# Kernel optimization log

Hardware: AMD Instinct MI355X
Metric: run time of the kernel (lower is better)

The kernel has to match this reference:

```python
import jax, jax.numpy as jnp
import numpy as np

N = 50000  # total nodes


def sage_conv(x, src, dst, Wl, Wr, b):
    # PyG SAGEConv with mean aggregation: out = mean_{j in N(i)} x_j @ Wl + x_i @ Wr + b
    agg = jax.ops.segment_sum(x[src], dst, num_segments=N)
    deg = jax.ops.segment_sum(jnp.ones((src.shape[0],), x.dtype), dst, num_segments=N)
    mean = agg / jnp.maximum(deg, 1.0)[:, None]
    return mean @ Wl + x @ Wr + b


def setup_inputs() -> dict:
    key = jax.random.key(0)
    ks = jax.random.split(key, 16)
    F_in, D, H, B, E1, E2, A = 128, 64, 128, 16, 800000, 200000, 2000
    s = lambda fan: 1.0 / np.sqrt(fan)
    return {
        "x": jax.random.normal(ks[0], (N, F_in), jnp.float32),
        "edge_index": jax.random.randint(ks[1], (2, E1), 0, N),
        "new_edges": jax.random.randint(ks[2], (B, 2, E2), 0, N),
        "target_nodes": jax.random.randint(ks[3], (B,), 0, N),
        "regions": jax.random.randint(ks[4], (B, A), 0, N),
        "W1l": jax.random.normal(ks[5], (F_in, D), jnp.float32) * s(F_in),
        "W1r": jax.random.normal(ks[6], (F_in, D), jnp.float32) * s(F_in),
        "b1": jnp.zeros((D,), jnp.float32),
        "W2l": jax.random.normal(ks[7], (D, D), jnp.float32) * s(D),
        "W2r": jax.random.normal(ks[8], (D, D), jnp.float32) * s(D),
        "b2": jnp.zeros((D,), jnp.float32),
        "Wm": jax.random.normal(ks[9], (D, H), jnp.float32) * s(D),
        "bm": jnp.zeros((H,), jnp.float32),
        "Wo": jax.random.normal(ks[10], (H, D), jnp.float32) * s(H),
        "bo": jnp.zeros((D,), jnp.float32),
    }


def reference(x, edge_index, new_edges, target_nodes, regions,
              W1l, W1r, b1, W2l, W2r, b2, Wm, bm, Wo, bo):
    # shared conv1 over base graph
    h1 = jax.nn.relu(sage_conv(x, edge_index[0], edge_index[1], W1l, W1r, b1))  # [N,D]

    def per_graph(edges, t, region):
        h2 = jax.nn.relu(sage_conv(h1, edges[0], edges[1], W2l, W2r, b2))  # [N,D]
        target_embed = h2[t]          # [D]
        region_embed = h2[region]     # [A,D]
        e = jax.nn.relu(region_embed @ Wm + bm)  # [A,H]
        r = e @ Wo + bo                           # [A,D]
        return r @ target_embed                   # [A]  (bilin_q)

    q = jax.vmap(per_graph)(new_edges, target_nodes, regions)  # [B,A]
    return q
```

## Files before the change

### kernel.cpp

```cpp
#include <hip/hip_runtime.h>
#include <hip/hip_bf16.h>

#define NN 50000
#define E1C 800000
#define E2C 200000
#define BC 16
#define AC 2000
#define FIN 128
#define DD 64
#define HH 128
#define SLOTS (AC + 1)
#define SCAP 64
#define SCAP2 32
#define NPART 8
#define PSZ (NN / NPART)

__global__ __launch_bounds__(256, 2) void k_lin1(const float* __restrict__ x,
    const float* __restrict__ W1l, const float* __restrict__ W1r,
    const float* __restrict__ b1,
    float* __restrict__ y, float* __restrict__ z) {
  __shared__ __align__(16) float Wsh[FIN][FIN];
  __shared__ __align__(16) float xr2[32][FIN];
  for (int i = threadIdx.x; i < FIN * FIN; i += 256) {
    int k = i >> 7, c = i & 127;
    Wsh[k][c] = (c < DD) ? W1l[k * DD + c] : W1r[k * DD + (c - DD)];
  }
  const int cg = threadIdx.x & 31, c0 = cg * 4;
  const int rg = threadIdx.x >> 5, r0 = rg * 4;
  float4 bias = make_float4(0.f, 0.f, 0.f, 0.f);
  if (cg >= 16) bias = *(const float4*)(b1 + c0 - DD);
  const int ntiles = (NN + 31) / 32;
  for (int t = blockIdx.x; t < ntiles; t += gridDim.x) {
    int base = t * 32;
    __syncthreads();
#pragma unroll
    for (int p = 0; p < 4; ++p) {
      int row = p * 8 + (threadIdx.x >> 5);
      int k0 = (threadIdx.x & 31) * 4;
      int gr = base + row;
      float4 v = (gr < NN) ? *(const float4*)(x + (size_t)gr * FIN + k0)
                           : make_float4(0.f, 0.f, 0.f, 0.f);
      *(float4*)&xr2[row][k0] = v;
    }
    __syncthreads();
    float acc[4][4] = {};
#pragma unroll 4
    for (int kk = 0; kk < FIN; kk += 4) {
      float4 xq0 = *(const float4*)&xr2[r0 + 0][kk];
      float4 xq1 = *(const float4*)&xr2[r0 + 1][kk];
      float4 xq2 = *(const float4*)&xr2[r0 + 2][kk];
      float4 xq3 = *(const float4*)&xr2[r0 + 3][kk];
#pragma unroll
      for (int j = 0; j < 4; ++j) {
        float4 wv = *(const float4*)&Wsh[kk + j][c0];
        float x0 = (j == 0) ? xq0.x : (j == 1) ? xq0.y : (j == 2) ? xq0.z : xq0.w;
        float x1 = (j == 0) ? xq1.x : (j == 1) ? xq1.y : (j == 2) ? xq1.z : xq1.w;
        float x2 = (j == 0) ? xq2.x : (j == 1) ? xq2.y : (j == 2) ? xq2.z : xq2.w;
        float x3 = (j == 0) ? xq3.x : (j == 1) ? xq3.y : (j == 2) ? xq3.z : xq3.w;
        acc[0][0] = fmaf(x0, wv.x, acc[0][0]); acc[0][1] = fmaf(x0, wv.y, acc[0][1]);
        acc[0][2] = fmaf(x0, wv.z, acc[0][2]); acc[0][3] = fmaf(x0, wv.w, acc[0][3]);
        acc[1][0] = fmaf(x1, wv.x, acc[1][0]); acc[1][1] = fmaf(x1, wv.y, acc[1][1]);
        acc[1][2] = fmaf(x1, wv.z, acc[1][2]); acc[1][3] = fmaf(x1, wv.w, acc[1][3]);
        acc[2][0] = fmaf(x2, wv.x, acc[2][0]); acc[2][1] = fmaf(x2, wv.y, acc[2][1]);
        acc[2][2] = fmaf(x2, wv.z, acc[2][2]); acc[2][3] = fmaf(x2, wv.w, acc[2][3]);
        acc[3][0] = fmaf(x3, wv.x, acc[3][0]); acc[3][1] = fmaf(x3, wv.y, acc[3][1]);
        acc[3][2] = fmaf(x3, wv.z, acc[3][2]); acc[3][3] = fmaf(x3, wv.w, acc[3][3]);
      }
    }
#pragma unroll
    for (int i = 0; i < 4; ++i) {
      int gr = base + r0 + i;
      if (gr < NN) {
        float4 o = make_float4(acc[i][0] + bias.x, acc[i][1] + bias.y,
                               acc[i][2] + bias.z, acc[i][3] + bias.w);
        if (cg < 16) *(float4*)(y + (size_t)gr * DD + c0) = o;
        else         *(float4*)(z + (size_t)gr * DD + (c0 - DD)) = o;
      }
    }
  }
}

__global__ __launch_bounds__(256) void k_degslot(const int* __restrict__ src,
    const int* __restrict__ dst, int* __restrict__ degi, int* __restrict__ slots) {
  int part = blockIdx.x & (NPART - 1);
  int lb   = blockIdx.x >> 3;
  int nlb  = gridDim.x >> 3;
  int lo = part * PSZ, hi = lo + PSZ;
  for (int e = lb * 256 + threadIdx.x; e < E1C; e += nlb * 256) {
    int d = dst[e];
    if (d >= lo && d < hi) {
      int p = atomicAdd(&degi[d], 1);
      if (p < SCAP) slots[(size_t)d * SCAP + p] = src[e];
    }
  }
}

__global__ __launch_bounds__(256) void k_gather_h1(const int* __restrict__ degi,
    const int* __restrict__ slots, const float* __restrict__ y,
    const float* __restrict__ z, float* __restrict__ h1) {
  int w = blockIdx.x * 4 + (threadIdx.x >> 6);
  int lane = threadIdx.x & 63;
  if (w >= NN) return;
  int deg = degi[w];
  int n = min(deg, SCAP);
  const int* sp = slots + (size_t)w * SCAP;
  float acc = 0.f;
  int j = 0;
  for (; j + 4 <= n; j += 4) {
    int s0 = sp[j], s1 = sp[j + 1], s2 = sp[j + 2], s3 = sp[j + 3];
    float a0 = y[(size_t)s0 * DD + lane];
    float a1 = y[(size_t)s1 * DD + lane];
    float a2 = y[(size_t)s2 * DD + lane];
    float a3 = y[(size_t)s3 * DD + lane];
    acc += (a0 + a1) + (a2 + a3);
  }
  for (; j < n; ++j) acc += y[(size_t)sp[j] * DD + lane];
  float m = acc / fmaxf((float)deg, 1.f);
  h1[(size_t)w * DD + lane] = fmaxf(m + z[(size_t)w * DD + lane], 0.f);
}

__global__ __launch_bounds__(256, 2) void k_lin2(const float* __restrict__ h1,
    const float* __restrict__ W2l, const float* __restrict__ W2r,
    const float* __restrict__ b2,
    float* __restrict__ u, float* __restrict__ v) {
  __shared__ __align__(16) float Wsh[DD][128];
  __shared__ __align__(16) float xr2[32][DD];
  for (int i = threadIdx.x; i < DD * 128; i += 256) {
    int k = i >> 7, c = i & 127;
    Wsh[k][c] = (c < DD) ? W2l[k * DD + c] : W2r[k * DD + (c - DD)];
  }
  const int cg = threadIdx.x & 31, c0 = cg * 4;
  const int rg = threadIdx.x >> 5, r0 = rg * 4;
  float4 bias = make_float4(0.f, 0.f, 0.f, 0.f);
  if (cg >= 16) bias = *(const float4*)(b2 + c0 - DD);
  const int ntiles = (NN + 31) / 32;
  for (int t = blockIdx.x; t < ntiles; t += gridDim.x) {
    int base = t * 32;
    __syncthreads();
#pragma unroll
    for (int p = 0; p < 2; ++p) {
      int row = p * 16 + (threadIdx.x >> 4);
      int k0 = (threadIdx.x & 15) * 4;
      int gr = base + row;
      float4 vv = (gr < NN) ? *(const float4*)(h1 + (size_t)gr * DD + k0)
                            : make_float4(0.f, 0.f, 0.f, 0.f);
      *(float4*)&xr2[row][k0] = vv;
    }
    __syncthreads();
    float acc[4][4] = {};
#pragma unroll 4
    for (int kk = 0; kk < DD; kk += 4) {
      float4 xq0 = *(const float4*)&xr2[r0 + 0][kk];
      float4 xq1 = *(const float4*)&xr2[r0 + 1][kk];
      float4 xq2 = *(const float4*)&xr2[r0 + 2][kk];
      float4 xq3 = *(const float4*)&xr2[r0 + 3][kk];
#pragma unroll
      for (int j = 0; j < 4; ++j) {
        float4 wv = *(const float4*)&Wsh[kk + j][c0];
        float x0 = (j == 0) ? xq0.x : (j == 1) ? xq0.y : (j == 2) ? xq0.z : xq0.w;
        float x1 = (j == 0) ? xq1.x : (j == 1) ? xq1.y : (j == 2) ? xq1.z : xq1.w;
        float x2 = (j == 0) ? xq2.x : (j == 1) ? xq2.y : (j == 2) ? xq2.z : xq2.w;
        float x3 = (j == 0) ? xq3.x : (j == 1) ? xq3.y : (j == 2) ? xq3.z : xq3.w;
        acc[0][0] = fmaf(x0, wv.x, acc[0][0]); acc[0][1] = fmaf(x0, wv.y, acc[0][1]);
        acc[0][2] = fmaf(x0, wv.z, acc[0][2]); acc[0][3] = fmaf(x0, wv.w, acc[0][3]);
        acc[1][0] = fmaf(x1, wv.x, acc[1][0]); acc[1][1] = fmaf(x1, wv.y, acc[1][1]);
        acc[1][2] = fmaf(x1, wv.z, acc[1][2]); acc[1][3] = fmaf(x1, wv.w, acc[1][3]);
        acc[2][0] = fmaf(x2, wv.x, acc[2][0]); acc[2][1] = fmaf(x2, wv.y, acc[2][1]);
        acc[2][2] = fmaf(x2, wv.z, acc[2][2]); acc[2][3] = fmaf(x2, wv.w, acc[2][3]);
        acc[3][0] = fmaf(x3, wv.x, acc[3][0]); acc[3][1] = fmaf(x3, wv.y, acc[3][1]);
        acc[3][2] = fmaf(x3, wv.z, acc[3][2]); acc[3][3] = fmaf(x3, wv.w, acc[3][3]);
      }
    }
#pragma unroll
    for (int i = 0; i < 4; ++i) {
      int gr = base + r0 + i;
      if (gr < NN) {
        float4 o = make_float4(acc[i][0] + bias.x, acc[i][1] + bias.y,
                               acc[i][2] + bias.z, acc[i][3] + bias.w);
        if (cg < 16) *(float4*)(u + (size_t)gr * DD + c0) = o;
        else         *(float4*)(v + (size_t)gr * DD + (c0 - DD)) = o;
      }
    }
  }
}

__global__ void k_mark(const int* __restrict__ regions, const int* __restrict__ targets,
                       int* __restrict__ mark, int* __restrict__ rep) {
  int i = blockIdx.x * blockDim.x + threadIdx.x;
  if (i >= BC * SLOTS) return;
  int b = i / SLOTS, k = i % SLOTS;
  int node = (k < AC) ? regions[b * AC + k] : targets[b];
  int old = atomicCAS(&mark[b * NN + node], -1, k);
  rep[i] = (old < 0) ? k : old;
}

__global__ void k_filter(const int* __restrict__ ne, const int* __restrict__ mark,
                         int* __restrict__ deg2i, int* __restrict__ slots2) {
  int e = blockIdx.x * blockDim.x + threadIdx.x;
  int b = blockIdx.y;
  if (e >= E2C) return;
  int d = ne[b * 2 * E2C + E2C + e];
  int k = mark[b * NN + d];
  if (k >= 0) {
    int s = ne[b * 2 * E2C + e];
    int p = atomicAdd(&deg2i[b * SLOTS + k], 1);
    if (p < SCAP2) slots2[((size_t)b * SLOTS + k) * SCAP2 + p] = s;
  }
}

__global__ __launch_bounds__(256) void k_gather_h2(const int* __restrict__ deg2i,
    const int* __restrict__ slots2, const int* __restrict__ rep,
    const int* __restrict__ regions, const int* __restrict__ targets,
    const float* __restrict__ u, const float* __restrict__ v,
    float* __restrict__ h2c) {
  int w = blockIdx.x * 4 + (threadIdx.x >> 6);
  int lane = threadIdx.x & 63;
  if (w >= BC * SLOTS) return;
  int b = w / SLOTS, k = w - b * SLOTS;
  int r = rep[w];
  int deg = deg2i[b * SLOTS + r];
  int n = min(deg, SCAP2);
  const int* sp = slots2 + ((size_t)b * SLOTS + r) * SCAP2;
  float acc = 0.f;
  int j = 0;
  for (; j + 4 <= n; j += 4) {
    int s0 = sp[j], s1 = sp[j + 1], s2 = sp[j + 2], s3 = sp[j + 3];
    float a0 = u[(size_t)s0 * DD + lane];
    float a1 = u[(size_t)s1 * DD + lane];
    float a2 = u[(size_t)s2 * DD + lane];
    float a3 = u[(size_t)s3 * DD + lane];
    acc += (a0 + a1) + (a2 + a3);
  }
  for (; j < n; ++j) acc += u[(size_t)sp[j] * DD + lane];
  int node = (k < AC) ? regions[b * AC + k] : targets[b];
  float m = acc / fmaxf((float)deg, 1.f);
  h2c[(size_t)w * DD + lane] = fmaxf(m + v[(size_t)node * DD + lane], 0.f);
}

__global__ void k_wt(const float* __restrict__ h2c, const float* __restrict__ Wo,
                     const float* __restrict__ bo, float* __restrict__ wt,
                     float* __restrict__ c0) {
  int b = blockIdx.x;
  int t = threadIdx.x;
  __shared__ float te[DD];
  if (t < DD) te[t] = h2c[((size_t)b * SLOTS + AC) * DD + t];
  __syncthreads();
  float acc = 0.f;
#pragma unroll
  for (int d = 0; d < DD; ++d) acc = fmaf(Wo[t * DD + d], te[d], acc);
  wt[b * HH + t] = acc;
  if (t == 0) {
    float s = 0.f;
    for (int d = 0; d < DD; ++d) s += bo[d] * te[d];
    c0[b] = s;
  }
}

__global__ __launch_bounds__(256) void k_q(const float* __restrict__ h2c,
    const float* __restrict__ Wm, const float* __restrict__ bm,
    const float* __restrict__ wt, const float* __restrict__ c0,
    float* __restrict__ q) {
  __shared__ float W[DD][HH];
  __shared__ float bmL[HH], wtL[HH];
  int b = blockIdx.y;
  for (int i = threadIdx.x; i < DD * HH; i += 256) W[i >> 7][i & 127] = Wm[i];
  if (threadIdx.x < HH) {
    bmL[threadIdx.x] = bm[threadIdx.x];
    wtL[threadIdx.x] = wt[b * HH + threadIdx.x];
  }
  __syncthreads();
  float cc = c0[b];
  int lane = threadIdx.x & 63;
  int wv = threadIdx.x >> 6;
  int nwv = (blockDim.x >> 6) * gridDim.x;
  for (int a = blockIdx.x * 4 + wv; a < AC; a += nwv) {
    float hv = h2c[((size_t)b * SLOTS + a) * DD + lane];
    float a0 = 0.f, a1 = 0.f;
#pragma unroll
    for (int d = 0; d < DD; ++d) {
      float xd = __shfl(hv, d);
      a0 = fmaf(xd, W[d][lane], a0);
      a1 = fmaf(xd, W[d][lane + 64], a1);
    }
    float e0 = fmaxf(a0 + bmL[lane], 0.f);
    float e1 = fmaxf(a1 + bmL[lane + 64], 0.f);
    float p = fmaf(e0, wtL[lane], e1 * wtL[lane + 64]);
#pragma unroll
    for (int m = 32; m; m >>= 1) p += __shfl_xor(p, m);
    if (lane == 0) q[b * AC + a] = p + cc;
  }
}

extern "C" void kernel_launch(void* const* d_in, const int* in_sizes, int n_in,
                              void* d_out, int out_size, void* d_ws, size_t ws_size,
                              hipStream_t stream) {
  const float* x    = (const float*)d_in[0];
  const int*   ei   = (const int*)d_in[1];
  const int*   ne   = (const int*)d_in[2];
  const int*   tgt  = (const int*)d_in[3];
  const int*   reg  = (const int*)d_in[4];
  const float* W1l  = (const float*)d_in[5];
  const float* W1r  = (const float*)d_in[6];
  const float* b1   = (const float*)d_in[7];
  const float* W2l  = (const float*)d_in[8];
  const float* W2r  = (const float*)d_in[9];
  const float* b2   = (const float*)d_in[10];
  const float* Wm   = (const float*)d_in[11];
  const float* bm   = (const float*)d_in[12];
  const float* Wo   = (const float*)d_in[13];
  const float* bo   = (const float*)d_in[14];
  float* q = (float*)d_out;

  char* w = (char*)d_ws;
  size_t off = 0;
  auto alloc = [&](size_t bytes) { void* p = w + off; off = (off + bytes + 255) & ~(size_t)255; return p; };
  float* y_u   = (float*)alloc((size_t)NN * DD * 4);
  float* z_v   = (float*)alloc((size_t)NN * DD * 4);
  float* h1b   = (float*)alloc((size_t)NN * DD * 4);
  int*   degi  = (int*)alloc((size_t)NN * 4);
  int*   slots = (int*)alloc((size_t)NN * SCAP * 4);
  int*   mark  = (int*)alloc((size_t)BC * NN * 4);
  int*   rep   = (int*)alloc((size_t)BC * SLOTS * 4);
  int*   deg2i = (int*)alloc((size_t)BC * SLOTS * 4);
  int*   slots2= (int*)alloc((size_t)BC * SLOTS * SCAP2 * 4);
  float* h2c   = (float*)alloc((size_t)BC * SLOTS * DD * 4);
  float* wt    = (float*)alloc((size_t)BC * HH * 4);
  float* c0    = (float*)alloc(64);
  (void)ws_size; (void)n_in; (void)in_sizes; (void)out_size;

  hipMemsetAsync(degi,  0,    (size_t)NN * 4, stream);
  hipMemsetAsync(mark,  0xFF, (size_t)BC * NN * 4, stream);
  hipMemsetAsync(deg2i, 0,    (size_t)BC * SLOTS * 4, stream);

  const int* e_src = ei;
  const int* e_dst = ei + E1C;

  k_lin1<<<512, 256, 0, stream>>>(x, W1l, W1r, b1, y_u, z_v);
  k_degslot<<<2048, 256, 0, stream>>>(e_src, e_dst, degi, slots);
  k_gather_h1<<<(NN + 3) / 4, 256, 0, stream>>>(degi, slots, y_u, z_v, h1b);
  k_lin2<<<512, 256, 0, stream>>>(h1b, W2l, W2r, b2, y_u, z_v);
  k_mark<<<(BC * SLOTS + 255) / 256, 256, 0, stream>>>(reg, tgt, mark, rep);
  k_filter<<<dim3((E2C + 255) / 256, BC), 256, 0, stream>>>(ne, mark, deg2i, slots2);
  k_gather_h2<<<(BC * SLOTS + 3) / 4, 256, 0, stream>>>(deg2i, slots2, rep, reg, tgt,
                                                        y_u, z_v, h2c);
  k_wt<<<BC, 128, 0, stream>>>(h2c, Wo, bo, wt, c0);
  k_q<<<dim3(32, BC), 256, 0, stream>>>(h2c, Wm, bm, wt, c0, q);
}
```

Baseline: 320.7 us.

## Merge independent kernels into combined launches and drop LDS staging in linears

Result: no change. 317.9 us (-0.9%).

```diff
diff --git a/kernel.cpp b/kernel.cpp
--- a/kernel.cpp
+++ b/kernel.cpp
@@ -14,13 +14,17 @@
 #define SCAP2 32
 #define NPART 8
 #define PSZ (NN / NPART)
+#define DEGB 2048
+#define MARKB ((BC * SLOTS + 255) / 256)
+#define GH1B ((NN + 3) / 4)
+#define FILTB 196
+#define Q_NBLK 32
 
 __global__ __launch_bounds__(256, 2) void k_lin1(const float* __restrict__ x,
     const float* __restrict__ W1l, const float* __restrict__ W1r,
     const float* __restrict__ b1,
     float* __restrict__ y, float* __restrict__ z) {
   __shared__ __align__(16) float Wsh[FIN][FIN];
-  __shared__ __align__(16) float xr2[32][FIN];
   for (int i = threadIdx.x; i < FIN * FIN; i += 256) {
     int k = i >> 7, c = i & 127;
     Wsh[k][c] = (c < DD) ? W1l[k * DD + c] : W1r[k * DD + (c - DD)];
@@ -29,27 +33,22 @@
   const int rg = threadIdx.x >> 5, r0 = rg * 4;
   float4 bias = make_float4(0.f, 0.f, 0.f, 0.f);
   if (cg >= 16) bias = *(const float4*)(b1 + c0 - DD);
+  __syncthreads();
   const int ntiles = (NN + 31) / 32;
   for (int t = blockIdx.x; t < ntiles; t += gridDim.x) {
     int base = t * 32;
-    __syncthreads();
-#pragma unroll
-    for (int p = 0; p < 4; ++p) {
-      int row = p * 8 + (threadIdx.x >> 5);
-      int k0 = (threadIdx.x & 31) * 4;
-      int gr = base + row;
-      float4 v = (gr < NN) ? *(const float4*)(x + (size_t)gr * FIN + k0)
-                           : make_float4(0.f, 0.f, 0.f, 0.f);
-      *(float4*)&xr2[row][k0] = v;
-    }
-    __syncthreads();
+    int gr0 = base + r0;
+    const float* xp0 = x + (size_t)min(gr0 + 0, NN - 1) * FIN;
+    const float* xp1 = x + (size_t)min(gr0 + 1, NN - 1) * FIN;
+    const float* xp2 = x + (size_t)min(gr0 + 2, NN - 1) * FIN;
+    const float* xp3 = x + (size_t)min(gr0 + 3, NN - 1) * FIN;
     float acc[4][4] = {};
 #pragma unroll 4
     for (int kk = 0; kk < FIN; kk += 4) {
-      float4 xq0 = *(const float4*)&xr2[r0 + 0][kk];
-      float4 xq1 = *(const float4*)&xr2[r0 + 1][kk];
-      float4 xq2 = *(const float4*)&xr2[r0 + 2][kk];
-      float4 xq3 = *(const float4*)&xr2[r0 + 3][kk];
+      float4 xq0 = *(const float4*)(xp0 + kk);
+      float4 xq1 = *(const float4*)(xp1 + kk);
+      float4 xq2 = *(const float4*)(xp2 + kk);
+      float4 xq3 = *(const float4*)(xp3 + kk);
 #pragma unroll
       for (int j = 0; j < 4; ++j) {
         float4 wv = *(const float4*)&Wsh[kk + j][c0];
@@ -80,51 +79,83 @@
   }
 }
 
-__global__ __launch_bounds__(256) void k_degslot(const int* __restrict__ src,
-    const int* __restrict__ dst, int* __restrict__ degi, int* __restrict__ slots) {
-  int part = blockIdx.x & (NPART - 1);
-  int lb   = blockIdx.x >> 3;
-  int nlb  = gridDim.x >> 3;
-  int lo = part * PSZ, hi = lo + PSZ;
-  for (int e = lb * 256 + threadIdx.x; e < E1C; e += nlb * 256) {
-    int d = dst[e];
-    if (d >= lo && d < hi) {
-      int p = atomicAdd(&degi[d], 1);
-      if (p < SCAP) slots[(size_t)d * SCAP + p] = src[e];
-    }
-  }
-}
-
-__global__ __launch_bounds__(256) void k_gather_h1(const int* __restrict__ degi,
+__global__ __launch_bounds__(256) void k_prep(const int* __restrict__ src,
+    const int* __restrict__ dst, int* __restrict__ degi, int* __restrict__ slots,
+    const int* __restrict__ regions, const int* __restrict__ targets,
+    int* __restrict__ mark, int* __restrict__ rep) {
+  if (blockIdx.x < DEGB) {
+    int part = blockIdx.x & (NPART - 1);
+    int lb   = blockIdx.x >> 3;
+    int nlb  = DEGB >> 3;
+    int lo = part * PSZ, hi = lo + PSZ;
+    for (int e = lb * 256 + threadIdx.x; e < E1C; e += nlb * 256) {
+      int d = dst[e];
+      if (d >= lo && d < hi) {
+        int p = atomicAdd(&degi[d], 1);
+        if (p < SCAP) slots[(size_t)d * SCAP + p] = src[e];
+      }
+    }
+  } else {
+    int i = (blockIdx.x - DEGB) * 256 + threadIdx.x;
+    if (i >= BC * SLOTS) return;
+    int b = i / SLOTS, k = i % SLOTS;
+    int node = (k < AC) ? regions[b * AC + k] : targets[b];
+    int old = atomicCAS(&mark[b * NN + node], -1, k);
+    rep[i] = (old < 0) ? k : old;
+  }
+}
+
+__global__ __launch_bounds__(256) void k_sparse2(const int* __restrict__ degi,
     const int* __restrict__ slots, const float* __restrict__ y,
-    const float* __restrict__ z, float* __restrict__ h1) {
-  int w = blockIdx.x * 4 + (threadIdx.x >> 6);
-  int lane = threadIdx.x & 63;
-  if (w >= NN) return;
-  int deg = degi[w];
-  int n = min(deg, SCAP);
-  const int* sp = slots + (size_t)w * SCAP;
-  float acc = 0.f;
-  int j = 0;
-  for (; j + 4 <= n; j += 4) {
-    int s0 = sp[j], s1 = sp[j + 1], s2 = sp[j + 2], s3 = sp[j + 3];
-    float a0 = y[(size_t)s0 * DD + lane];
-    float a1 = y[(size_t)s1 * DD + lane];
-    float a2 = y[(size_t)s2 * DD + lane];
-    float a3 = y[(size_t)s3 * DD + lane];
-    acc += (a0 + a1) + (a2 + a3);
-  }
-  for (; j < n; ++j) acc += y[(size_t)sp[j] * DD + lane];
-  float m = acc / fmaxf((float)deg, 1.f);
-  h1[(size_t)w * DD + lane] = fmaxf(m + z[(size_t)w * DD + lane], 0.f);
-}
-
-__global__ __launch_bounds__(256, 2) void k_lin2(const float* __restrict__ h1,
+    const float* __restrict__ z, float* __restrict__ h1,
+    const int* __restrict__ ne, const int* __restrict__ mark,
+    int* __restrict__ deg2i, int* __restrict__ slots2) {
+  if (blockIdx.x < GH1B) {
+    int w = blockIdx.x * 4 + (threadIdx.x >> 6);
+    int lane = threadIdx.x & 63;
+    if (w >= NN) return;
+    int deg = degi[w];
+    int n = min(deg, SCAP);
+    const int* sp = slots + (size_t)w * SCAP;
+    float acc = 0.f;
+    int j = 0;
+    for (; j + 4 <= n; j += 4) {
+      int s0 = sp[j], s1 = sp[j + 1], s2 = sp[j + 2], s3 = sp[j + 3];
+      float a0 = y[(size_t)s0 * DD + lane];
+      float a1 = y[(size_t)s1 * DD + lane];
+      float a2 = y[(size_t)s2 * DD + lane];
+      float a3 = y[(size_t)s3 * DD + lane];
+      acc += (a0 + a1) + (a2 + a3);
+    }
+    for (; j < n; ++j) acc += y[(size_t)sp[j] * DD + lane];
+    float m = acc / fmaxf((float)deg, 1.f);
+    h1[(size_t)w * DD + lane] = fmaxf(m + z[(size_t)w * DD + lane], 0.f);
+  } else {
+    int fid = blockIdx.x - GH1B;
+    int b = fid / FILTB, eb = fid % FILTB;
+    int e = eb * 1024 + threadIdx.x * 4;
+    if (e >= E2C) return;
+    const int* srcp = ne + (size_t)b * 2 * E2C;
+    const int* dstp = srcp + E2C;
+    int4 d4 = *(const int4*)(dstp + e);
+    const int* mb = mark + (size_t)b * NN;
+    int k0 = mb[d4.x], k1 = mb[d4.y], k2 = mb[d4.z], k3 = mb[d4.w];
+    if (k0 >= 0) { int p = atomicAdd(&deg2i[b * SLOTS + k0], 1);
+      if (p < SCAP2) slots2[((size_t)b * SLOTS + k0) * SCAP2 + p] = srcp[e]; }
+    if (k1 >= 0) { int p = atomicAdd(&deg2i[b * SLOTS + k1], 1);
+      if (p < SCAP2) slots2[((size_t)b * SLOTS + k1) * SCAP2 + p] = srcp[e + 1]; }
+    if (k2 >= 0) { int p = atomicAdd(&deg2i[b * SLOTS + k2], 1);
+      if (p < SCAP2) slots2[((size_t)b * SLOTS + k2) * SCAP2 + p] = srcp[e + 2]; }
+    if (k3 >= 0) { int p = atomicAdd(&deg2i[b * SLOTS + k3], 1);
+      if (p < SCAP2) slots2[((size_t)b * SLOTS + k3) * SCAP2 + p] = srcp[e + 3]; }
+  }
+}
+
+__global__ __launch_bounds__(256, 4) void k_lin2(const float* __restrict__ h1,
     const float* __restrict__ W2l, const float* __restrict__ W2r,
     const float* __restrict__ b2,
     float* __restrict__ u, float* __restrict__ v) {
   __shared__ __align__(16) float Wsh[DD][128];
-  __shared__ __align__(16) float xr2[32][DD];
   for (int i = threadIdx.x; i < DD * 128; i += 256) {
     int k = i >> 7, c = i & 127;
     Wsh[k][c] = (c < DD) ? W2l[k * DD + c] : W2r[k * DD + (c - DD)];
@@ -133,27 +164,22 @@
   const int rg = threadIdx.x >> 5, r0 = rg * 4;
   float4 bias = make_float4(0.f, 0.f, 0.f, 0.f);
   if (cg >= 16) bias = *(const float4*)(b2 + c0 - DD);
+  __syncthreads();
   const int ntiles = (NN + 31) / 32;
   for (int t = blockIdx.x; t < ntiles; t += gridDim.x) {
     int base = t * 32;
-    __syncthreads();
-#pragma unroll
-    for (int p = 0; p < 2; ++p) {
-      int row = p * 16 + (threadIdx.x >> 4);
-      int k0 = (threadIdx.x & 15) * 4;
-      int gr = base + row;
-      float4 vv = (gr < NN) ? *(const float4*)(h1 + (size_t)gr * DD + k0)
-                            : make_float4(0.f, 0.f, 0.f, 0.f);
-      *(float4*)&xr2[row][k0] = vv;
-    }
-    __syncthreads();
+    int gr0 = base + r0;
+    const float* xp0 = h1 + (size_t)min(gr0 + 0, NN - 1) * DD;
+    const float* xp1 = h1 + (size_t)min(gr0 + 1, NN - 1) * DD;
+    const float* xp2 = h1 + (size_t)min(gr0 + 2, NN - 1) * DD;
+    const float* xp3 = h1 + (size_t)min(gr0 + 3, NN - 1) * DD;
     float acc[4][4] = {};
 #pragma unroll 4
     for (int kk = 0; kk < DD; kk += 4) {
-      float4 xq0 = *(const float4*)&xr2[r0 + 0][kk];
-      float4 xq1 = *(const float4*)&xr2[r0 + 1][kk];
-      float4 xq2 = *(const float4*)&xr2[r0 + 2][kk];
-      float4 xq3 = *(const float4*)&xr2[r0 + 3][kk];
+      float4 xq0 = *(const float4*)(xp0 + kk);
+      float4 xq1 = *(const float4*)(xp1 + kk);
+      float4 xq2 = *(const float4*)(xp2 + kk);
+      float4 xq3 = *(const float4*)(xp3 + kk);
 #pragma unroll
       for (int j = 0; j < 4; ++j) {
         float4 wv = *(const float4*)&Wsh[kk + j][c0];
@@ -181,30 +207,6 @@
         else         *(float4*)(v + (size_t)gr * DD + (c0 - DD)) = o;
       }
     }
-  }
-}
-
-__global__ void k_mark(const int* __restrict__ regions, const int* __restrict__ targets,
-                       int* __restrict__ mark, int* __restrict__ rep) {
-  int i = blockIdx.x * blockDim.x + threadIdx.x;
-  if (i >= BC * SLOTS) return;
-  int b = i / SLOTS, k = i % SLOTS;
-  int node = (k < AC) ? regions[b * AC + k] : targets[b];
-  int old = atomicCAS(&mark[b * NN + node], -1, k);
-  rep[i] = (old < 0) ? k : old;
-}
-
-__global__ void k_filter(const int* __restrict__ ne, const int* __restrict__ mark,
-                         int* __restrict__ deg2i, int* __restrict__ slots2) {
-  int e = blockIdx.x * blockDim.x + threadIdx.x;
-  int b = blockIdx.y;
-  if (e >= E2C) return;
-  int d = ne[b * 2 * E2C + E2C + e];
-  int k = mark[b * NN + d];
-  if (k >= 0) {
-    int s = ne[b * 2 * E2C + e];
-    int p = atomicAdd(&deg2i[b * SLOTS + k], 1);
-    if (p < SCAP2) slots2[((size_t)b * SLOTS + k) * SCAP2 + p] = s;
   }
 }
 
@@ -237,39 +239,30 @@
   h2c[(size_t)w * DD + lane] = fmaxf(m + v[(size_t)node * DD + lane], 0.f);
 }
 
-__global__ void k_wt(const float* __restrict__ h2c, const float* __restrict__ Wo,
-                     const float* __restrict__ bo, float* __restrict__ wt,
-                     float* __restrict__ c0) {
-  int b = blockIdx.x;
-  int t = threadIdx.x;
-  __shared__ float te[DD];
-  if (t < DD) te[t] = h2c[((size_t)b * SLOTS + AC) * DD + t];
+__global__ __launch_bounds__(256) void k_q(const float* __restrict__ h2c,
+    const float* __restrict__ Wm, const float* __restrict__ bm,
+    const float* __restrict__ Wo, const float* __restrict__ bo,
+    float* __restrict__ q) {
+  __shared__ float W[DD][HH];
+  __shared__ float bmL[HH], wtL[HH], te[DD];
+  __shared__ float c0s;
+  int b = blockIdx.y;
+  for (int i = threadIdx.x; i < DD * HH; i += 256) W[i >> 7][i & 127] = Wm[i];
+  if (threadIdx.x < HH) bmL[threadIdx.x] = bm[threadIdx.x];
+  if (threadIdx.x < DD) te[threadIdx.x] = h2c[((size_t)b * SLOTS + AC) * DD + threadIdx.x];
   __syncthreads();
-  float acc = 0.f;
-#pragma unroll
-  for (int d = 0; d < DD; ++d) acc = fmaf(Wo[t * DD + d], te[d], acc);
-  wt[b * HH + t] = acc;
-  if (t == 0) {
+  if (threadIdx.x < HH) {
+    float a = 0.f;
+#pragma unroll
+    for (int d = 0; d < DD; ++d) a = fmaf(Wo[threadIdx.x * DD + d], te[d], a);
+    wtL[threadIdx.x] = a;
+  } else if (threadIdx.x == HH) {
     float s = 0.f;
     for (int d = 0; d < DD; ++d) s += bo[d] * te[d];
-    c0[b] = s;
-  }
-}
-
-__global__ __launch_bounds__(256) void k_q(const float* __restrict__ h2c,
-    const float* __restrict__ Wm, const float* __restrict__ bm,
-    const float* __restrict__ wt, const float* __restrict__ c0,
-    float* __restrict__ q) {
-  __shared__ float W[DD][HH];
-  __shared__ float bmL[HH], wtL[HH];
-  int b = blockIdx.y;
-  for (int i = threadIdx.x; i < DD * HH; i += 256) W[i >> 7][i & 127] = Wm[i];
-  if (threadIdx.x < HH) {
-    bmL[threadIdx.x] = bm[threadIdx.x];
-    wtL[threadIdx.x] = wt[b * HH + threadIdx.x];
+    c0s = s;
   }
   __syncthreads();
-  float cc = c0[b];
+  float cc = c0s;
   int lane = threadIdx.x & 63;
   int wv = threadIdx.x >> 6;
   int nwv = (blockDim.x >> 6) * gridDim.x;
@@ -324,8 +317,6 @@
   int*   deg2i = (int*)alloc((size_t)BC * SLOTS * 4);
   int*   slots2= (int*)alloc((size_t)BC * SLOTS * SCAP2 * 4);
   float* h2c   = (float*)alloc((size_t)BC * SLOTS * DD * 4);
-  float* wt    = (float*)alloc((size_t)BC * HH * 4);
-  float* c0    = (float*)alloc(64);
   (void)ws_size; (void)n_in; (void)in_sizes; (void)out_size;
 
   hipMemsetAsync(degi,  0,    (size_t)NN * 4, stream);
@@ -336,13 +327,11 @@
   const int* e_dst = ei + E1C;
 
   k_lin1<<<512, 256, 0, stream>>>(x, W1l, W1r, b1, y_u, z_v);
-  k_degslot<<<2048, 256, 0, stream>>>(e_src, e_dst, degi, slots);
-  k_gather_h1<<<(NN + 3) / 4, 256, 0, stream>>>(degi, slots, y_u, z_v, h1b);
-  k_lin2<<<512, 256, 0, stream>>>(h1b, W2l, W2r, b2, y_u, z_v);
-  k_mark<<<(BC * SLOTS + 255) / 256, 256, 0, stream>>>(reg, tgt, mark, rep);
-  k_filter<<<dim3((E2C + 255) / 256, BC), 256, 0, stream>>>(ne, mark, deg2i, slots2);
+  k_prep<<<DEGB + MARKB, 256, 0, stream>>>(e_src, e_dst, degi, slots, reg, tgt, mark, rep);
+  k_sparse2<<<GH1B + BC * FILTB, 256, 0, stream>>>(degi, slots, y_u, z_v, h1b,
+                                                   ne, mark, deg2i, slots2);
+  k_lin2<<<1024, 256, 0, stream>>>(h1b, W2l, W2r, b2, y_u, z_v);
   k_gather_h2<<<(BC * SLOTS + 3) / 4, 256, 0, stream>>>(deg2i, slots2, rep, reg, tgt,
                                                         y_u, z_v, h2c);
-  k_wt<<<BC, 128, 0, stream>>>(h2c, Wo, bo, wt, c0);
-  k_q<<<dim3(32, BC), 256, 0, stream>>>(h2c, Wm, bm, wt, c0, q);
-}
+  k_q<<<dim3(Q_NBLK, BC), 256, 0, stream>>>(h2c, Wm, bm, Wo, bo, q);
+}
```
